# Kernel optimization log

Hardware: AMD Instinct MI355X
Metric: run time of the kernel (lower is better)

## Reference

```python
import jax, jax.numpy as jnp
import numpy as np

SEQ_LEN, BATCH, NUM_TAGS = 512, 1024, 64


def setup_inputs() -> dict:
    key = jax.random.key(0)
    k_em, k_tag, k_st, k_en, k_tr = jax.random.split(key, 5)
    return {
        "emissions": jax.random.normal(k_em, (SEQ_LEN, BATCH, NUM_TAGS), jnp.float32),
        "tags": jax.random.randint(k_tag, (SEQ_LEN, BATCH), 0, NUM_TAGS),
        "mask": jnp.ones((SEQ_LEN, BATCH), jnp.bool_),
        "start_transitions": jax.random.uniform(k_st, (NUM_TAGS,), jnp.float32, -0.1, 0.1),
        "end_transitions": jax.random.uniform(k_en, (NUM_TAGS,), jnp.float32, -0.1, 0.1),
        "transitions": jax.random.uniform(k_tr, (NUM_TAGS, NUM_TAGS), jnp.float32, -0.1, 0.1),
    }


def reference(emissions, tags, mask, start_transitions, end_transitions, transitions):
    # emissions: (L, B, T) float; tags/mask: (L, B)
    L, B, T = emissions.shape
    mf = mask.astype(emissions.dtype)

    # ---- numerator: joint log-likelihood of the gold tag path ----
    e_scores = jnp.take_along_axis(emissions, tags[..., None], axis=2)[..., 0]  # (L, B)
    num = start_transitions[tags[0]]                                   # (B,)
    num = num + jnp.sum(e_scores[:-1] * mf[:-1], axis=0)               # emissions at t=0..L-2
    num = num + jnp.sum(transitions[tags[:-1], tags[1:]] * mf[1:], axis=0)
    last_idx = mask.astype(jnp.int32).sum(axis=0) - 1                  # (B,)
    barange = jnp.arange(B)
    last_tags = tags[last_idx, barange]                                # (B,)
    num = num + end_transitions[last_tags] + emissions[-1, barange, last_tags] * mf[-1]

    # ---- denominator: log partition via forward-algorithm scan ----
    alpha0 = start_transitions[None, :] + emissions[0]                 # (B, T)

    def step(alpha, xs):
        e_i, m_i = xs  # (B, T), (B,)
        # (B, cur_tag, next_tag) broadcast-add then logsumexp over cur_tag
        score = alpha[:, :, None] + transitions[None, :, :] + e_i[:, None, :]
        new = jax.nn.logsumexp(score, axis=1)
        return jnp.where(m_i[:, None], new, alpha), None

    alpha, _ = jax.lax.scan(step, alpha0, (emissions[1:], mask[1:]))
    log_z = jax.nn.logsumexp(alpha + end_transitions[None, :], axis=1)  # (B,)

    # reduce=True: sum over batch
    return jnp.sum(num - log_z)
```

## Files before the change

### kernel.cpp

```cpp
#include <hip/hip_runtime.h>


constexpr int L = 512;
constexpr int B = 1024;
constexpr int T = 64;

typedef _Float16 h2 __attribute__((ext_vector_type(2)));

#if defined(__has_builtin)
#if __has_builtin(__builtin_amdgcn_fdot2)
#define USE_FDOT2 1
#else
#define USE_FDOT2 0
#endif
#else
#define USE_FDOT2 0
#endif

__global__ __launch_bounds__(64, 1) __attribute__((amdgpu_waves_per_eu(1, 1)))
void crf_kernel(const float* __restrict__ em,
                const int*   __restrict__ tags,
                const float* __restrict__ st,
                const float* __restrict__ en,
                const float* __restrict__ tr,
                float* __restrict__ out)
{
    const int lane = threadIdx.x;
    const int b    = blockIdx.x;

#if USE_FDOT2
    h2 Ef[32];
    #pragma unroll
    for (int k = 0; k < 32; ++k) {
        h2 v;
        v.x = (_Float16)__expf(tr[(2 * k)     * T + lane]);
        v.y = (_Float16)__expf(tr[(2 * k + 1) * T + lane]);
        Ef[k] = v;
    }
#else
    float Ee[64];
    #pragma unroll
    for (int i = 0; i < 64; ++i)
        Ee[i] = __expf(tr[i * T + lane]);
#endif

    const size_t row_off = (size_t)b * T + lane;

    float alpha0 = st[lane] + em[row_off];
    float C  = __builtin_bit_cast(float,
                 __builtin_amdgcn_readfirstlane(__builtin_bit_cast(int, alpha0)));
    float pt = __expf(alpha0 - C);

    float ering[8];
    #pragma unroll
    for (int j = 0; j < 8; ++j)
        ering[j] = em[(size_t)(1 + j) * B * T + row_off];

    auto step = [&](float e_cur) {
        float p0  = __builtin_bit_cast(float,
                      __builtin_amdgcn_readfirstlane(__builtin_bit_cast(int, pt)));
        float g64 = 64.0f * p0;
        float u   = 1.0f / g64;
        C += __logf(g64);
        float w = __expf(e_cur) * u;

#if USE_FDOT2
        int   ptb = __builtin_bit_cast(int, pt);
        int   nbb = __builtin_amdgcn_update_dpp(0, ptb, 0xB1, 0xF, 0xF, true);
        float ptn = __builtin_bit_cast(float, nbb);
        int   ppb = __builtin_bit_cast(int, __builtin_amdgcn_cvt_pkrtz(pt, ptn));
        float a[4] = {0.f, 0.f, 0.f, 0.f};
        #pragma unroll
        for (int k = 0; k < 32; ++k) {
            h2 pv = __builtin_bit_cast(h2, __builtin_amdgcn_readlane(ppb, 2 * k));
            a[k & 3] = __builtin_amdgcn_fdot2(pv, Ef[k], a[k & 3], false);
        }
#else
        int ptb = __builtin_bit_cast(int, pt);
        float a[4] = {0.f, 0.f, 0.f, 0.f};
        #pragma unroll
        for (int i = 0; i < 64; ++i) {
            float pv = __builtin_bit_cast(float, __builtin_amdgcn_readlane(ptb, i));
            a[i & 3] = __builtin_fmaf(pv, Ee[i], a[i & 3]);
        }
#endif
        float s = (a[0] + a[1]) + (a[2] + a[3]);
        pt = s * w;
    };

    int t = 1;
    for (int blk = 0; blk < 63; ++blk) {
        #pragma unroll
        for (int j = 0; j < 8; ++j) {
            float e_cur = ering[j];
            int tn = t + 8;
            if (tn > L - 1) tn = L - 1;
            ering[j] = em[(size_t)tn * B * T + row_off];
            step(e_cur);
            ++t;
        }
    }
    #pragma unroll
    for (int j = 0; j < 7; ++j) {
        step(ering[j]);
        ++t;
    }

    float v = pt * __expf(en[lane]);
    #pragma unroll
    for (int off = 32; off > 0; off >>= 1)
        v += __shfl_xor(v, off, 64);
    float log_z = C + __logf(v);

    int tagv[8];
    #pragma unroll
    for (int r = 0; r < 8; ++r)
        tagv[r] = tags[(size_t)(r * 64 + lane) * B + b];
    float ev[8];
    #pragma unroll
    for (int r = 0; r < 8; ++r)
        ev[r] = em[(size_t)(r * 64 + lane) * B * T + (size_t)b * T + tagv[r]];

    float nsum = 0.f;
    int carry = 0;
    #pragma unroll
    for (int r = 0; r < 8; ++r) {
        int tag = tagv[r];
        int tp  = __shfl_up(tag, 1, 64);
        if (lane == 0) tp = carry;
        nsum += ev[r];
        if (r == 0 && lane == 0)
            nsum += st[tag];
        else
            nsum += tr[tp * T + tag];
        carry = __shfl(tag, 63, 64);
    }
    if (lane == 63) nsum += en[tagv[7]];
    #pragma unroll
    for (int off = 32; off > 0; off >>= 1)
        nsum += __shfl_xor(nsum, off, 64);

    if (lane == 0)
        atomicAdd(out, nsum - log_z);
}

extern "C" void kernel_launch(void* const* d_in, const int* in_sizes, int n_in,
                              void* d_out, int out_size, void* d_ws, size_t ws_size,
                              hipStream_t stream) {
    const float* em   = (const float*)d_in[0];
    const int*   tags = (const int*)d_in[1];
    const float* st   = (const float*)d_in[3];
    const float* en   = (const float*)d_in[4];
    const float* tr   = (const float*)d_in[5];
    float* out = (float*)d_out;

    hipMemsetAsync(out, 0, sizeof(float), stream);
    crf_kernel<<<B, 64, 0, stream>>>(em, tags, st, en, tr, out);
}
```

Before: 288.3 us.

## Batch 16 sequences per wave and compute forward recursion with MFMA

```diff
diff --git a/kernel.cpp b/kernel.cpp
--- a/kernel.cpp
+++ b/kernel.cpp
@@ -4,113 +4,147 @@
 constexpr int L = 512;
 constexpr int B = 1024;
 constexpr int T = 64;
+constexpr int BT = B * T;
 
-typedef _Float16 h2 __attribute__((ext_vector_type(2)));
+typedef _Float16 h4 __attribute__((ext_vector_type(4)));
+typedef float    f4 __attribute__((ext_vector_type(4)));
+typedef int      i2 __attribute__((ext_vector_type(2)));
 
-#if defined(__has_builtin)
-#if __has_builtin(__builtin_amdgcn_fdot2)
-#define USE_FDOT2 1
-#else
-#define USE_FDOT2 0
-#endif
-#else
-#define USE_FDOT2 0
-#endif
+__device__ __forceinline__ h4 pack4_rtz(float a, float b, float c, float d) {
+    i2 p;
+    p.x = __builtin_bit_cast(int, __builtin_amdgcn_cvt_pkrtz(a, b));
+    p.y = __builtin_bit_cast(int, __builtin_amdgcn_cvt_pkrtz(c, d));
+    return __builtin_bit_cast(h4, p);
+}
 
-__global__ __launch_bounds__(64, 1) __attribute__((amdgpu_waves_per_eu(1, 1)))
-void crf_kernel(const float* __restrict__ em,
-                const int*   __restrict__ tags,
-                const float* __restrict__ st,
-                const float* __restrict__ en,
-                const float* __restrict__ tr,
-                float* __restrict__ out)
+__device__ __forceinline__ f4 exp4(f4 v) {
+    f4 r;
+    r.x = __expf(v.x); r.y = __expf(v.y);
+    r.z = __expf(v.z); r.w = __expf(v.w);
+    return r;
+}
+
+__global__ __launch_bounds__(64, 1)
+void crf_forward(const float* __restrict__ em,
+                 const float* __restrict__ st,
+                 const float* __restrict__ en,
+                 const float* __restrict__ tr,
+                 float* __restrict__ out)
 {
     const int lane = threadIdx.x;
-    const int b    = blockIdx.x;
+    const int s = lane & 15;
+    const int g = lane >> 4;
+    const int b0 = blockIdx.x * 16;
 
-#if USE_FDOT2
-    h2 Ef[32];
+    h4 A[4][4];
     #pragma unroll
-    for (int k = 0; k < 32; ++k) {
-        h2 v;
-        v.x = (_Float16)__expf(tr[(2 * k)     * T + lane]);
-        v.y = (_Float16)__expf(tr[(2 * k + 1) * T + lane]);
-        Ef[k] = v;
+    for (int m = 0; m < 4; ++m) {
+        #pragma unroll
+        for (int k = 0; k < 4; ++k) {
+            const float* t0 = tr + (16 * k + 4 * g) * T + 16 * m + s;
+            h4 a;
+            a.x = (_Float16)__expf(t0[0 * T]);
+            a.y = (_Float16)__expf(t0[1 * T]);
+            a.z = (_Float16)__expf(t0[2 * T]);
+            a.w = (_Float16)__expf(t0[3 * T]);
+            A[m][k] = a;
+        }
     }
-#else
-    float Ee[64];
-    #pragma unroll
-    for (int i = 0; i < 64; ++i)
-        Ee[i] = __expf(tr[i * T + lane]);
-#endif
 
-    const size_t row_off = (size_t)b * T + lane;
+    const size_t off0 = (size_t)(b0 + s) * T + 4 * g;
 
-    float alpha0 = st[lane] + em[row_off];
-    float C  = __builtin_bit_cast(float,
-                 __builtin_amdgcn_readfirstlane(__builtin_bit_cast(int, alpha0)));
-    float pt = __expf(alpha0 - C);
+    float C = 0.f;
+    h4 Bf[4];
+    f4 pt[4];
 
-    float ering[8];
-    #pragma unroll
-    for (int j = 0; j < 8; ++j)
-        ering[j] = em[(size_t)(1 + j) * B * T + row_off];
-
-    auto step = [&](float e_cur) {
-        float p0  = __builtin_bit_cast(float,
-                      __builtin_amdgcn_readfirstlane(__builtin_bit_cast(int, pt)));
-        float g64 = 64.0f * p0;
-        float u   = 1.0f / g64;
-        C += __logf(g64);
-        float w = __expf(e_cur) * u;
-
-#if USE_FDOT2
-        int   ptb = __builtin_bit_cast(int, pt);
-        int   nbb = __builtin_amdgcn_update_dpp(0, ptb, 0xB1, 0xF, 0xF, true);
-        float ptn = __builtin_bit_cast(float, nbb);
-        int   ppb = __builtin_bit_cast(int, __builtin_amdgcn_cvt_pkrtz(pt, ptn));
-        float a[4] = {0.f, 0.f, 0.f, 0.f};
+    auto norm_pack = [&]() {
+        f4 t4 = (pt[0] + pt[1]) + (pt[2] + pt[3]);
+        float ssum = (t4.x + t4.y) + (t4.z + t4.w);
+        ssum += __shfl_xor(ssum, 16, 64);
+        ssum += __shfl_xor(ssum, 32, 64);
+        float u = __builtin_amdgcn_rcpf(ssum);
+        C += __logf(ssum);
         #pragma unroll
-        for (int k = 0; k < 32; ++k) {
-            h2 pv = __builtin_bit_cast(h2, __builtin_amdgcn_readlane(ppb, 2 * k));
-            a[k & 3] = __builtin_amdgcn_fdot2(pv, Ef[k], a[k & 3], false);
-        }
-#else
-        int ptb = __builtin_bit_cast(int, pt);
-        float a[4] = {0.f, 0.f, 0.f, 0.f};
-        #pragma unroll
-        for (int i = 0; i < 64; ++i) {
-            float pv = __builtin_bit_cast(float, __builtin_amdgcn_readlane(ptb, i));
-            a[i & 3] = __builtin_fmaf(pv, Ee[i], a[i & 3]);
-        }
-#endif
-        float s = (a[0] + a[1]) + (a[2] + a[3]);
-        pt = s * w;
+        for (int m = 0; m < 4; ++m)
+            Bf[m] = pack4_rtz(pt[m].x * u, pt[m].y * u,
+                              pt[m].z * u, pt[m].w * u);
     };
 
-    int t = 1;
-    for (int blk = 0; blk < 63; ++blk) {
+    #pragma unroll
+    for (int m = 0; m < 4; ++m) {
+        f4 stv = *reinterpret_cast<const f4*>(st + 16 * m + 4 * g);
+        f4 e0  = *reinterpret_cast<const f4*>(em + off0 + 16 * m);
+        pt[m] = exp4(stv + e0);
+    }
+    norm_pack();
+
+    f4 er[4][4];
+    const float* pld  = em + (size_t)1 * BT + off0;
+    const float* plim = em + (size_t)(L - 1) * BT + off0;
+    #pragma unroll
+    for (int j = 0; j < 4; ++j) {
         #pragma unroll
-        for (int j = 0; j < 8; ++j) {
-            float e_cur = ering[j];
-            int tn = t + 8;
-            if (tn > L - 1) tn = L - 1;
-            ering[j] = em[(size_t)tn * B * T + row_off];
-            step(e_cur);
-            ++t;
+        for (int m = 0; m < 4; ++m)
+            er[j][m] = *reinterpret_cast<const f4*>(pld + 16 * m);
+        pld += BT;
+    }
+
+    auto stepf = [&](f4 (&e)[4], const float* pl) {
+        f4 w[4];
+        #pragma unroll
+        for (int m = 0; m < 4; ++m) {
+            f4 ev = e[m];
+            if (pl)
+                e[m] = *reinterpret_cast<const f4*>(pl + 16 * m);
+            w[m] = exp4(ev);
+        }
+        #pragma unroll
+        for (int m = 0; m < 4; ++m) {
+            f4 c = {0.f, 0.f, 0.f, 0.f};
+            #pragma unroll
+            for (int k = 0; k < 4; ++k)
+                c = __builtin_amdgcn_mfma_f32_16x16x16f16(A[m][k], Bf[k], c,
+                                                          0, 0, 0);
+            pt[m] = c * w[m];
+        }
+    };
+
+    for (int blk = 0; blk < 127; ++blk) {
+        #pragma unroll
+        for (int j = 0; j < 4; ++j) {
+            const float* p = (pld > plim) ? plim : pld;
+            stepf(er[j], p);
+            pld += BT;
+            norm_pack();
         }
     }
+    stepf(er[0], nullptr); norm_pack();
+    stepf(er[1], nullptr); norm_pack();
+    stepf(er[2], nullptr);
+
+    f4 z4 = {0.f, 0.f, 0.f, 0.f};
     #pragma unroll
-    for (int j = 0; j < 7; ++j) {
-        step(ering[j]);
-        ++t;
+    for (int m = 0; m < 4; ++m) {
+        f4 env = *reinterpret_cast<const f4*>(en + 16 * m + 4 * g);
+        z4 += pt[m] * exp4(env);
     }
-
-    float v = pt * __expf(en[lane]);
+    float z = (z4.x + z4.y) + (z4.z + z4.w);
+    z += __shfl_xor(z, 16, 64);
+    z += __shfl_xor(z, 32, 64);
+    float val = (lane < 16) ? -(C + __logf(z)) : 0.f;
     #pragma unroll
     for (int off = 32; off > 0; off >>= 1)
-        v += __shfl_xor(v, off, 64);
-    float log_z = C + __logf(v);
+        val += __shfl_xor(val, off, 64);
+    if (lane == 0) atomicAdd(out, val);
+}
+
+__global__ __launch_bounds__(64, 1)
+void crf_numer(const float* __restrict__ em, const int* __restrict__ tags,
+               const float* __restrict__ st, const float* __restrict__ en,
+               const float* __restrict__ tr, float* __restrict__ out)
+{
+    const int lane = threadIdx.x;
+    const int b = blockIdx.x;
 
     int tagv[8];
     #pragma unroll
@@ -119,14 +153,14 @@
     float ev[8];
     #pragma unroll
     for (int r = 0; r < 8; ++r)
-        ev[r] = em[(size_t)(r * 64 + lane) * B * T + (size_t)b * T + tagv[r]];
+        ev[r] = em[(size_t)(r * 64 + lane) * BT + (size_t)b * T + tagv[r]];
 
     float nsum = 0.f;
     int carry = 0;
     #pragma unroll
     for (int r = 0; r < 8; ++r) {
         int tag = tagv[r];
-        int tp  = __shfl_up(tag, 1, 64);
+        int tp = __shfl_up(tag, 1, 64);
         if (lane == 0) tp = carry;
         nsum += ev[r];
         if (r == 0 && lane == 0)
@@ -139,9 +173,7 @@
     #pragma unroll
     for (int off = 32; off > 0; off >>= 1)
         nsum += __shfl_xor(nsum, off, 64);
-
-    if (lane == 0)
-        atomicAdd(out, nsum - log_z);
+    if (lane == 0) atomicAdd(out, nsum);
 }
 
 extern "C" void kernel_launch(void* const* d_in, const int* in_sizes, int n_in,
@@ -155,5 +187,6 @@
     float* out = (float*)d_out;
 
     hipMemsetAsync(out, 0, sizeof(float), stream);
-    crf_kernel<<<B, 64, 0, stream>>>(em, tags, st, en, tr, out);
+    crf_forward<<<64, 64, 0, stream>>>(em, st, en, tr, out);
+    crf_numer<<<B, 64, 0, stream>>>(em, tags, st, en, tr, out);
 }
```

Result: slower. 541.3 us (+87.8%).
